# Kernel optimization log

Hardware: AMD Instinct MI355X
Metric: run time of the kernel (lower is better)

## Reference

```python
import jax, jax.numpy as jnp
import numpy as np

HID, NHEAD, NLAYERS = 128, 8, 6
BS, H, W = 1, 64, 128
HD = HID // NHEAD  # head dim = 16


def layer_norm(x, g, b, eps=1e-5):
    m = jnp.mean(x, -1, keepdims=True)
    v = jnp.mean((x - m) ** 2, -1, keepdims=True)
    return (x - m) * jax.lax.rsqrt(v + eps) * g + b


def mha_relative(query, kv, in_w, in_b, out_w, out_b, pos_enc, pos_idx, attn_mask, is_self):
    # query/kv: [W, N, C]; in_w: [3C, C]; pos_enc: [2W-1, C]; pos_idx: [W*W]
    w, n, c = query.shape
    if is_self:
        q, k, v = jnp.split(query @ in_w.T + in_b, 3, axis=-1)
    else:
        q = query @ in_w[:c].T + in_b[:c]
        k, v = jnp.split(kv @ in_w[c:].T + in_b[c:], 2, axis=-1)
    # relative positional bias: gather [2W-1,C] -> [W,W,C], project with q/k weights
    pos_sel = pos_enc[pos_idx].reshape(w, w, c)
    q_r, k_r = jnp.split(pos_sel @ in_w[:2 * c].T + in_b[:2 * c], 2, axis=-1)
    scale = HD ** -0.5
    q = (q * scale).reshape(w, n, NHEAD, HD)
    k = k.reshape(w, n, NHEAD, HD)
    v = v.reshape(w, n, NHEAD, HD)
    q_r = (q_r * scale).reshape(w, w, NHEAD, HD)
    k_r = k_r.reshape(w, w, NHEAD, HD)
    attn = (jnp.einsum('wnec,vnec->newv', q, k)
            + jnp.einsum('wnec,wvec->newv', q, k_r)
            + jnp.einsum('vnec,wvec->newv', k, q_r))  # [N,E,W,W]
    if attn_mask is not None:
        attn = attn + attn_mask[None, None]
    raw_attn = attn.sum(axis=1)  # [N,W,W] head-summed raw scores
    a = jax.nn.softmax(attn, axis=-1)
    v_o = jnp.einsum('newv,vnec->wnec', a, v).reshape(w, n, c)
    return v_o @ out_w.T + out_b, raw_attn


def setup_inputs() -> dict:
    key = jax.random.key(0)
    ks = jax.random.split(key, 8)
    f32 = jnp.float32
    s = 0.02
    d = {}
    d['feat_left'] = jax.random.normal(ks[0], (BS, HID, H, W), f32)
    d['feat_right'] = jax.random.normal(ks[1], (BS, HID, H, W), f32)
    d['pos_enc'] = jax.random.normal(ks[2], (2 * W - 1, HID), f32)
    d['self_ln_g'] = jnp.ones((NLAYERS, HID), f32)
    d['self_ln_b'] = jnp.zeros((NLAYERS, HID), f32)
    d['self_in_w'] = jax.random.normal(ks[3], (NLAYERS, 3 * HID, HID), f32) * s
    d['self_in_b'] = jnp.zeros((NLAYERS, 3 * HID), f32)
    d['self_out_w'] = jax.random.normal(ks[4], (NLAYERS, HID, HID), f32) * s
    d['self_out_b'] = jnp.zeros((NLAYERS, HID), f32)
    d['cross_ln1_g'] = jnp.ones((NLAYERS, HID), f32)
    d['cross_ln1_b'] = jnp.zeros((NLAYERS, HID), f32)
    d['cross_ln2_g'] = jnp.ones((NLAYERS, HID), f32)
    d['cross_ln2_b'] = jnp.zeros((NLAYERS, HID), f32)
    d['cross_in_w'] = jax.random.normal(ks[5], (NLAYERS, 3 * HID, HID), f32) * s
    d['cross_in_b'] = jnp.zeros((NLAYERS, 3 * HID), f32)
    d['cross_out_w'] = jax.random.normal(ks[6], (NLAYERS, HID, HID), f32) * s
    d['cross_out_b'] = jnp.zeros((NLAYERS, HID), f32)
    return d


def reference(feat_left, feat_right, pos_enc, self_ln_g, self_ln_b, self_in_w, self_in_b,
              self_out_w, self_out_b, cross_ln1_g, cross_ln1_b, cross_ln2_g, cross_ln2_b,
              cross_in_w, cross_in_b, cross_out_w, cross_out_b):
    bs, c, hn, w = feat_left.shape  # bs must be 1 (as in source)
    # [N,C,H,W] -> [W, H*N, C]
    fl = jnp.transpose(feat_left, (3, 2, 0, 1)).reshape(w, hn * bs, c)
    fr = jnp.transpose(feat_right, (3, 2, 0, 1)).reshape(w, hn * bs, c)
    HN = hn * bs
    # pos_indexes[i,j] = (w-1-i) + j, values in [0, 2w-2]
    pos_idx = ((w - 1 - jnp.arange(w))[:, None] + jnp.arange(w)[None, :]).reshape(-1)
    causal = jnp.triu(jnp.full((w, w), -jnp.inf, feat_left.dtype), k=1)
    feat = jnp.concatenate([fl, fr], axis=1)  # [W, 2HN, C]
    raw_attn = None
    for i in range(NLAYERS):
        # self attention over concatenated left+right rows
        f2 = layer_norm(feat, self_ln_g[i], self_ln_b[i])
        upd, _ = mha_relative(f2, f2, self_in_w[i], self_in_b[i], self_out_w[i],
                              self_out_b[i], pos_enc, pos_idx, None, True)
        feat = feat + upd
        left, right = feat[:, :HN], feat[:, HN:]
        # cross attention: left queries attend to norm2(right)
        # (source computes a right-update with norm1/flipped pos but discards it)
        l2 = layer_norm(left, cross_ln1_g[i], cross_ln1_b[i])
        r2 = layer_norm(right, cross_ln2_g[i], cross_ln2_b[i])
        mask = causal if i == NLAYERS - 1 else None
        upd, raw_attn = mha_relative(l2, r2, cross_in_w[i], cross_in_b[i], cross_out_w[i],
                                     cross_out_b[i], pos_enc, pos_idx, mask, False)
        left = left + upd
        feat = jnp.concatenate([left, right], axis=1)
    # [HN,W,W] -> [bs, hn, W, W]
    return jnp.transpose(raw_attn.reshape(hn, bs, w, w), (1, 0, 2, 3))
```

## Files before the change

### kernel.cpp

```cpp
#include <hip/hip_runtime.h>
#include <cmath>

#define CDIM 128

typedef __attribute__((ext_vector_type(8))) short bf16x8;
typedef __attribute__((ext_vector_type(4))) float f32x4;
typedef unsigned short u16;

__device__ inline unsigned pk2(float a, float b) {
    unsigned ua = __float_as_uint(a) + 0x8000u;
    unsigned ub = __float_as_uint(b) + 0x8000u;
    return (ua >> 16) | (ub & 0xffff0000u);
}
__device__ inline u16 pk1(float x) {
    return (u16)((__float_as_uint(x) + 0x8000u) >> 16);
}
__device__ inline float ubf(u16 u) { return __uint_as_float(((unsigned)u) << 16); }
__device__ inline float ulo(unsigned u) { return __uint_as_float(u << 16); }
__device__ inline float uhi(unsigned u) { return __uint_as_float(u & 0xffff0000u); }

__global__ __launch_bounds__(256) void setup1_kernel(const float* __restrict__ w0,
                                                     const float* __restrict__ w1,
                                                     const float* __restrict__ w2,
                                                     const float* __restrict__ w3,
                                                     const float* __restrict__ b0,
                                                     const float* __restrict__ b1,
                                                     u16* __restrict__ wout,
                                                     float* __restrict__ bout,
                                                     const float* __restrict__ FL,
                                                     const float* __restrict__ FR,
                                                     u16* __restrict__ feat) {
    __shared__ float t[32][33];
    int bb = blockIdx.x;
    if (bb < 786) {
        int idx = bb * 256 + threadIdx.x;
        if (idx < 196608) {
            const float* src; long off4; u16* dst;
            if (idx < 73728)       { src = w0; off4 = idx;           dst = wout; }
            else if (idx < 147456) { src = w1; off4 = idx - 73728;   dst = wout + 294912; }
            else if (idx < 172032) { src = w2; off4 = idx - 147456;  dst = wout + 589824; }
            else                   { src = w3; off4 = idx - 172032;  dst = wout + 688128; }
            float4 f = *(const float4*)(src + off4 * 4);
            *(uint2*)(dst + off4 * 4) = make_uint2(pk2(f.x, f.y), pk2(f.z, f.w));
        } else {
            int tt = idx - 196608;
            if (tt < 4608) bout[tt] = (tt < 2304) ? b0[tt] : b1[tt - 2304];
        }
        return;
    }
    int b = bb - 786;
    int cb = b & 3, wb = (b >> 2) & 3, n = b >> 4;
    const float* src = (n < 64) ? FL : FR;
    int nn = n & 63;
    int j = threadIdx.x & 31, i0 = threadIdx.x >> 5;
    #pragma unroll
    for (int p = 0; p < 4; p++) {
        int i = i0 + p * 8;
        t[i][j] = src[(cb * 32 + i) * 8192 + nn * 128 + wb * 32 + j];
    }
    __syncthreads();
    #pragma unroll
    for (int p = 0; p < 4; p++) {
        int i = i0 + p * 8;
        feat[((long)(wb * 32 + i) * 128 + n) * 128 + cb * 32 + j] = pk1(t[j][i]);
    }
}

__global__ __launch_bounds__(256, 4) void setup2_kernel(const u16* __restrict__ feat,
                                                        const float* __restrict__ g,
                                                        const float* __restrict__ b,
                                                        u16* __restrict__ lnB,
                                                        const float* __restrict__ Apos,
                                                        const u16* __restrict__ Wpp,
                                                        const float* __restrict__ biaspp,
                                                        u16* __restrict__ Cpp,
                                                        float scale) {
    __shared__ __align__(16) u16 sA[64 * 136];
    __shared__ __align__(16) u16 sW[64 * 136];
    int bb = blockIdx.x;
    int tid = threadIdx.x;
    if (bb < 1024) {
        int wv = tid >> 6, lane = tid & 63;
        float g0 = g[lane * 2], b0 = b[lane * 2];
        float g1 = g[lane * 2 + 1], b1 = b[lane * 2 + 1];
        #pragma unroll
        for (int rr = 0; rr < 4; rr++) {
            long m = (long)bb * 16 + wv * 4 + rr;
            unsigned u = *(const unsigned*)(feat + m * 128 + lane * 2);
            float x0 = ulo(u), x1 = uhi(u);
            float s = x0 + x1, q = x0 * x0 + x1 * x1;
            #pragma unroll
            for (int off = 1; off < 64; off <<= 1) {
                s += __shfl_xor(s, off);
                q += __shfl_xor(q, off);
            }
            float mean = s * (1.f / 128.f);
            float var = q * (1.f / 128.f) - mean * mean;
            float rs = rsqrtf(var + 1e-5f);
            float y0 = (x0 - mean) * rs * g0 + b0;
            float y1 = (x1 - mean) * rs * g1 + b1;
            *(unsigned*)(lnB + m * 128 + lane * 2) = pk2(y0, y1);
        }
        return;
    }
    int b2 = bb - 1024;
    int bx = b2 & 3, byy = (b2 >> 2) & 3, z = b2 >> 4;
    const int M = 255, N = 256;
    const u16* W = Wpp + (long)z * 49152;
    const float* bias = biaspp + z * 384;
    u16* C = Cpp + (long)z * 65280;
    int row0 = byy * 64, col0 = bx * 64;
    float4 zf4 = make_float4(0.f, 0.f, 0.f, 0.f);
    int kc = tid & 31;
    #pragma unroll
    for (int i = 0; i < 8; i++) {
        int r = (tid + i * 256) >> 5;
        int m = row0 + r;
        int jn = col0 + r;
        float4 fa = (m < M) ? *(const float4*)(Apos + (long)m * 128 + kc * 4) : zf4;
        uint2 uw = make_uint2(0u, 0u);
        if (jn < N) uw = *(const uint2*)(W + (long)jn * 128 + kc * 4);
        *(uint2*)&sA[r * 136 + kc * 4] = make_uint2(pk2(fa.x, fa.y), pk2(fa.z, fa.w));
        *(uint2*)&sW[r * 136 + kc * 4] = uw;
    }
    __syncthreads();

    int wv = tid >> 6, lane = tid & 63, quad = lane >> 4, col = lane & 15;
    f32x4 z4 = {0.f, 0.f, 0.f, 0.f};
    f32x4 acc0 = z4, acc1 = z4, acc2 = z4, acc3 = z4;
    #pragma unroll
    for (int kb = 0; kb < 4; kb++) {
        bf16x8 a = *(const bf16x8*)&sA[(wv * 16 + col) * 136 + kb * 32 + quad * 8];
        bf16x8 b0 = *(const bf16x8*)&sW[(0 * 16 + col) * 136 + kb * 32 + quad * 8];
        bf16x8 b1 = *(const bf16x8*)&sW[(1 * 16 + col) * 136 + kb * 32 + quad * 8];
        bf16x8 b2 = *(const bf16x8*)&sW[(2 * 16 + col) * 136 + kb * 32 + quad * 8];
        bf16x8 b3 = *(const bf16x8*)&sW[(3 * 16 + col) * 136 + kb * 32 + quad * 8];
        acc0 = __builtin_amdgcn_mfma_f32_16x16x32_bf16(a, b0, acc0, 0, 0, 0);
        acc1 = __builtin_amdgcn_mfma_f32_16x16x32_bf16(a, b1, acc1, 0, 0, 0);
        acc2 = __builtin_amdgcn_mfma_f32_16x16x32_bf16(a, b2, acc2, 0, 0, 0);
        acc3 = __builtin_amdgcn_mfma_f32_16x16x32_bf16(a, b3, acc3, 0, 0, 0);
    }
    int mrow = row0 + wv * 16 + quad * 4;
    #pragma unroll
    for (int tc = 0; tc < 4; tc++) {
        f32x4 acc = tc == 0 ? acc0 : tc == 1 ? acc1 : tc == 2 ? acc2 : acc3;
        int jn = col0 + tc * 16 + col;
        if (jn >= N) continue;
        float bs = bias[jn];
        float sc = (jn < 128) ? scale : 1.f;
        long db = ((long)(jn >> 4) * 255) * 16 + (jn & 15);
        #pragma unroll
        for (int reg = 0; reg < 4; reg++) {
            int m = mrow + reg;
            if (m >= M) continue;
            C[db + (long)m * 16] = pk1((acc[reg] + bs) * sc);
        }
    }
}

__global__ __launch_bounds__(256, 3) void gemm_qkv128_kernel(const u16* __restrict__ A,
                                                             const u16* __restrict__ W,
                                                             const float* __restrict__ bias,
                                                             u16* __restrict__ C,
                                                             float scale) {
    __shared__ __align__(16) u16 sA[128 * 136];
    __shared__ __align__(16) u16 sW[64 * 136];
    int tid = threadIdx.x;
    int row0 = blockIdx.y * 128, col0 = blockIdx.x * 64;
    int kc = tid & 31;
    #pragma unroll
    for (int i = 0; i < 16; i++) {
        int r = (tid + i * 256) >> 5;
        *(uint2*)&sA[r * 136 + kc * 4] =
            *(const uint2*)(A + (long)(row0 + r) * 128 + kc * 4);
    }
    #pragma unroll
    for (int i = 0; i < 8; i++) {
        int r = (tid + i * 256) >> 5;
        *(uint2*)&sW[r * 136 + kc * 4] =
            *(const uint2*)(W + (long)(col0 + r) * 128 + kc * 4);
    }
    __syncthreads();

    int wv = tid >> 6, lane = tid & 63, quad = lane >> 4, col = lane & 15;
    f32x4 z4 = {0.f, 0.f, 0.f, 0.f};
    f32x4 accA0 = z4, accA1 = z4, accA2 = z4, accA3 = z4;
    f32x4 accB0 = z4, accB1 = z4, accB2 = z4, accB3 = z4;
    #pragma unroll
    for (int kb = 0; kb < 4; kb++) {
        bf16x8 a0 = *(const bf16x8*)&sA[(wv * 32 + col) * 136 + kb * 32 + quad * 8];
        bf16x8 a1 = *(const bf16x8*)&sA[(wv * 32 + 16 + col) * 136 + kb * 32 + quad * 8];
        bf16x8 b0 = *(const bf16x8*)&sW[(0 * 16 + col) * 136 + kb * 32 + quad * 8];
        bf16x8 b1 = *(const bf16x8*)&sW[(1 * 16 + col) * 136 + kb * 32 + quad * 8];
        bf16x8 b2 = *(const bf16x8*)&sW[(2 * 16 + col) * 136 + kb * 32 + quad * 8];
        bf16x8 b3 = *(const bf16x8*)&sW[(3 * 16 + col) * 136 + kb * 32 + quad * 8];
        accA0 = __builtin_amdgcn_mfma_f32_16x16x32_bf16(a0, b0, accA0, 0, 0, 0);
        accA1 = __builtin_amdgcn_mfma_f32_16x16x32_bf16(a0, b1, accA1, 0, 0, 0);
        accA2 = __builtin_amdgcn_mfma_f32_16x16x32_bf16(a0, b2, accA2, 0, 0, 0);
        accA3 = __builtin_amdgcn_mfma_f32_16x16x32_bf16(a0, b3, accA3, 0, 0, 0);
        accB0 = __builtin_amdgcn_mfma_f32_16x16x32_bf16(a1, b0, accB0, 0, 0, 0);
        accB1 = __builtin_amdgcn_mfma_f32_16x16x32_bf16(a1, b1, accB1, 0, 0, 0);
        accB2 = __builtin_amdgcn_mfma_f32_16x16x32_bf16(a1, b2, accB2, 0, 0, 0);
        accB3 = __builtin_amdgcn_mfma_f32_16x16x32_bf16(a1, b3, accB3, 0, 0, 0);
    }
    long woff = (long)blockIdx.y * 16;
    #pragma unroll
    for (int st = 0; st < 2; st++) {
        int nrow = wv * 32 + st * 16 + quad * 4;
        #pragma unroll
        for (int tc = 0; tc < 4; tc++) {
            f32x4 acc;
            if (st == 0) acc = tc == 0 ? accA0 : tc == 1 ? accA1 : tc == 2 ? accA2 : accA3;
            else         acc = tc == 0 ? accB0 : tc == 1 ? accB1 : tc == 2 ? accB2 : accB3;
            int jn = col0 + tc * 16 + col;
            float bs = bias[jn];
            float sc = (jn < 128) ? scale : 1.f;
            long db = ((long)(jn >> 4) * 128) * 2048 + woff + (jn & 15);
            #pragma unroll
            for (int reg = 0; reg < 4; reg++)
                C[db + (long)(nrow + reg) * 2048] = pk1((acc[reg] + bs) * sc);
        }
    }
}

__global__ __launch_bounds__(256, 2) void f1_out_self_cqkv_kernel(
        const u16* __restrict__ A,
        const u16* __restrict__ W,
        const float* __restrict__ bias,
        u16* __restrict__ feat,
        const float* __restrict__ g1, const float* __restrict__ b1,
        const float* __restrict__ g2, const float* __restrict__ b2,
        const float* __restrict__ sng, const float* __restrict__ snb,
        u16* __restrict__ lnB,
        const u16* __restrict__ Wcr,
        const float* __restrict__ biac,
        u16* __restrict__ QKV,
        float scale) {
    __shared__ __align__(16) u16 sA[64 * 136];
    __shared__ __align__(16) u16 sW[128 * 136];
    int tid = threadIdx.x;
    int by = blockIdx.x;
    int row0 = by * 64;
    int right = by & 1;
    int w = by >> 1;
    int kc = tid & 31;
    #pragma unroll
    for (int i = 0; i < 8; i++) {
        int r = (tid + i * 256) >> 5;
        *(uint2*)&sA[r * 136 + kc * 4] = *(const uint2*)(A + (long)(row0 + r) * 128 + kc * 4);
    }
    #pragma unroll
    for (int i = 0; i < 16; i++) {
        int r = (tid + i * 256) >> 5;
        *(uint2*)&sW[r * 136 + kc * 4] = *(const uint2*)(W + (long)r * 128 + kc * 4);
    }
    __syncthreads();

    int wv = tid >> 6, lane = tid & 63, quad = lane >> 4, col = lane & 15;
    f32x4 acc[8] = {};
    #pragma unroll
    for (int kb = 0; kb < 4; kb++) {
        bf16x8 a = *(const bf16x8*)&sA[(wv * 16 + col) * 136 + kb * 32 + quad * 8];
        #pragma unroll
        for (int tc = 0; tc < 8; tc++) {
            bf16x8 b = *(const bf16x8*)&sW[(tc * 16 + col) * 136 + kb * 32 + quad * 8];
            acc[tc] = __builtin_amdgcn_mfma_f32_16x16x32_bf16(a, b, acc[tc], 0, 0, 0);
        }
    }
    __syncthreads();

    const float* gA = right ? g2 : g1;
    const float* bA = right ? b2 : b1;
    float gAv[8], bAv[8], gBv[8], bBv[8], bsv[8];
    bool doB = (sng != nullptr) && right;
    #pragma unroll
    for (int tc = 0; tc < 8; tc++) {
        int jn = tc * 16 + col;
        gAv[tc] = gA[jn]; bAv[tc] = bA[jn]; bsv[tc] = bias[jn];
        if (doB) { gBv[tc] = sng[jn]; bBv[tc] = snb[jn]; }
    }
    #pragma unroll
    for (int reg = 0; reg < 4; reg++) {
        int nloc = wv * 16 + quad * 4 + reg;
        long m = row0 + nloc;
        long rb = m * 128;
        float o[8];
        float s = 0.f, q = 0.f;
        #pragma unroll
        for (int tc = 0; tc < 8; tc++) {
            int jn = tc * 16 + col;
            float v = acc[tc][reg] + bsv[tc] + ubf(feat[rb + jn]);
            o[tc] = v; s += v; q += v * v;
        }
        #pragma unroll
        for (int off = 1; off < 16; off <<= 1) {
            s += __shfl_xor(s, off);
            q += __shfl_xor(q, off);
        }
        float mean = s * (1.f / 128.f);
        float var = q * (1.f / 128.f) - mean * mean;
        float rs = rsqrtf(var + 1e-5f);
        #pragma unroll
        for (int tc = 0; tc < 8; tc++) {
            int jn = tc * 16 + col;
            feat[rb + jn] = pk1(o[tc]);
            float ln = (o[tc] - mean) * rs;
            sA[nloc * 136 + jn] = pk1(ln * gAv[tc] + bAv[tc]);
            if (doB) lnB[rb + jn] = pk1(ln * gBv[tc] + bBv[tc]);
        }
    }
    __syncthreads();

    int passes = right ? 2 : 1;
    for (int p = 0; p < passes; p++) {
        if (p) __syncthreads();
        int wrow0 = right ? (128 + p * 128) : 0;
        #pragma unroll
        for (int i = 0; i < 16; i++) {
            int r = (tid + i * 256) >> 5;
            *(uint2*)&sW[r * 136 + kc * 4] =
                *(const uint2*)(Wcr + (long)(wrow0 + r) * 128 + kc * 4);
        }
        __syncthreads();
        f32x4 acb[8] = {};
        #pragma unroll
        for (int kb = 0; kb < 4; kb++) {
            bf16x8 a = *(const bf16x8*)&sA[(wv * 16 + col) * 136 + kb * 32 + quad * 8];
            #pragma unroll
            for (int tc = 0; tc < 8; tc++) {
                bf16x8 b = *(const bf16x8*)&sW[(tc * 16 + col) * 136 + kb * 32 + quad * 8];
                acb[tc] = __builtin_amdgcn_mfma_f32_16x16x32_bf16(a, b, acb[tc], 0, 0, 0);
            }
        }
        float sc = right ? 1.f : scale;
        int nrow = wv * 16 + quad * 4;
        #pragma unroll
        for (int tc = 0; tc < 8; tc++) {
            int jn = tc * 16 + col;
            float bs = biac[wrow0 + jn];
            int strip = right ? (8 + p * 8 + (jn >> 4)) : (jn >> 4);
            long db = (long)strip * 131072 + w * 16 + (jn & 15);
            #pragma unroll
            for (int reg = 0; reg < 4; reg++)
                QKV[db + (long)(nrow + reg) * 2048] = pk1((acb[tc][reg] + bs) * sc);
        }
    }
}

__global__ __launch_bounds__(256, 3) void gemm_out_cross_kernel(const u16* __restrict__ A,
                                                                const u16* __restrict__ W,
                                                                const float* __restrict__ bias,
                                                                u16* __restrict__ feat,
                                                                const float* __restrict__ sng,
                                                                const float* __restrict__ snb,
                                                                u16* __restrict__ lnB) {
    __shared__ __align__(16) u16 sA[64 * 136];
    __shared__ __align__(16) u16 sW[128 * 136];
    int tid = threadIdx.x;
    int row0 = blockIdx.x * 64;
    int kc = tid & 31;
    #pragma unroll
    for (int i = 0; i < 8; i++) {
        int r = (tid + i * 256) >> 5;
        *(uint2*)&sA[r * 136 + kc * 4] = *(const uint2*)(A + (long)(row0 + r) * 128 + kc * 4);
    }
    #pragma unroll
    for (int i = 0; i < 16; i++) {
        int r = (tid + i * 256) >> 5;
        *(uint2*)&sW[r * 136 + kc * 4] = *(const uint2*)(W + (long)r * 128 + kc * 4);
    }
    __syncthreads();

    int wv = tid >> 6, lane = tid & 63, quad = lane >> 4, col = lane & 15;
    f32x4 acc[8] = {};
    #pragma unroll
    for (int kb = 0; kb < 4; kb++) {
        bf16x8 a = *(const bf16x8*)&sA[(wv * 16 + col) * 136 + kb * 32 + quad * 8];
        #pragma unroll
        for (int tc = 0; tc < 8; tc++) {
            bf16x8 b = *(const bf16x8*)&sW[(tc * 16 + col) * 136 + kb * 32 + quad * 8];
            acc[tc] = __builtin_amdgcn_mfma_f32_16x16x32_bf16(a, b, acc[tc], 0, 0, 0);
        }
    }
    float gBv[8], bBv[8], bsv[8];
    #pragma unroll
    for (int tc = 0; tc < 8; tc++) {
        int jn = tc * 16 + col;
        gBv[tc] = sng[jn]; bBv[tc] = snb[jn]; bsv[tc] = bias[jn];
    }
    #pragma unroll
    for (int reg = 0; reg < 4; reg++) {
        long m = row0 + wv * 16 + quad * 4 + reg;
        long rb = ((m >> 6) * 128 + (m & 63)) * 128;
        float o[8];
        float s = 0.f, q = 0.f;
        #pragma unroll
        for (int tc = 0; tc < 8; tc++) {
            int jn = tc * 16 + col;
            float v = acc[tc][reg] + bsv[tc] + ubf(feat[rb + jn]);
            o[tc] = v; s += v; q += v * v;
        }
        #pragma unroll
        for (int off = 1; off < 16; off <<= 1) {
            s += __shfl_xor(s, off);
            q += __shfl_xor(q, off);
        }
        float mean = s * (1.f / 128.f);
        float var = q * (1.f / 128.f) - mean * mean;
        float rs = rsqrtf(var + 1e-5f);
        #pragma unroll
        for (int tc = 0; tc < 8; tc++) {
            int jn = tc * 16 + col;
            feat[rb + jn] = pk1(o[tc]);
            lnB[rb + jn] = pk1((o[tc] - mean) * rs * gBv[tc] + bBv[tc]);
        }
    }
}

__global__ __launch_bounds__(512, 8) void attn_kernel(const u16* __restrict__ QKV,
                                                      const u16* __restrict__ PPL,
                                                      u16* __restrict__ VO,
                                                      float* __restrict__ RAW,
                                                      int NN, int causal) {
    __shared__ __align__(16) u16 sm[19584];
    const int SKV = 0, SA = 2176;
    int e = blockIdx.x, n = blockIdx.y;
    int tid = threadIdx.x;
    int wv = tid >> 6, lane = tid & 63, quad = lane >> 4, col = lane & 15;

    const u16* qb = QKV + ((long)e * NN + n) * 2048;
    const u16* kb = QKV + ((long)(8 + e) * NN + n) * 2048;
    const u16* vb = QKV + ((long)(16 + e) * NN + n) * 2048;
    const u16* qr = PPL + (long)e * 4080;
    const u16* kr = PPL + (long)(8 + e) * 4080;

    bf16x8 zf = {0, 0, 0, 0, 0, 0, 0, 0};
    f32x4 z4 = {0.f, 0.f, 0.f, 0.f};
    bf16x8 aQ = zf, aK = zf;
    if (quad < 2) {
        aQ = *(const bf16x8*)(qb + (wv * 16 + col) * 16 + quad * 8);
        aK = *(const bf16x8*)(kb + (wv * 16 + col) * 16 + quad * 8);
    }
    {
        int row = tid >> 2, c = tid & 3;
        *(uint2*)&sm[SKV + row * 16 + c * 4] = *(const uint2*)(kb + row * 16 + c * 4);
    }
    __syncthreads();

    f32x4 s1[8];
    #pragma unroll
    for (int tv = 0; tv < 8; tv++) {
        bf16x8 b = zf;
        if (quad < 2) b = *(const bf16x8*)&sm[SKV + (tv * 16 + col) * 16 + quad * 8];
        s1[tv] = __builtin_amdgcn_mfma_f32_16x16x32_bf16(aQ, b, z4, 0, 0, 0);
    }
    int wbq = wv * 16 + quad * 4;
    int s2lo = 7 - wv;
    #pragma unroll 3
    for (int tt = 0; tt < 9; tt++) {
        int tr = s2lo + tt;
        bf16x8 b = zf;
        if (quad < 2) b = *(const bf16x8*)(kr + (tr * 16 + col) * 16 + quad * 8);
        f32x4 d = __builtin_amdgcn_mfma_f32_16x16x32_bf16(aQ, b, z4, 0, 0, 0);
        #pragma unroll
        for (int reg = 0; reg < 4; reg++) {
            int v = tr * 16 + col - 127 + wbq + reg;
            if (v >= 0 && v < 128) sm[SA + (wbq + reg) * 136 + v] = pk1(d[reg]);
        }
    }
    __syncthreads();
    {
        int row = tid >> 2, c = tid & 3;
        uint2 uv = *(const uint2*)(vb + row * 16 + c * 4);
        sm[SKV + (c * 4 + 0) * 136 + row] = (u16)(uv.x & 0xffffu);
        sm[SKV + (c * 4 + 1) * 136 + row] = (u16)(uv.x >> 16);
        sm[SKV + (c * 4 + 2) * 136 + row] = (u16)(uv.y & 0xffffu);
        sm[SKV + (c * 4 + 3) * 136 + row] = (u16)(uv.y >> 16);
    }
    #pragma unroll 3
    for (int tt = 0; tt < 9; tt++) {
        int tr = wv + tt;
        bf16x8 b = zf;
        if (quad < 2) b = *(const bf16x8*)(qr + (tr * 16 + col) * 16 + quad * 8);
        f32x4 d = __builtin_amdgcn_mfma_f32_16x16x32_bf16(aK, b, z4, 0, 0, 0);
        #pragma unroll
        for (int reg = 0; reg < 4; reg++) {
            int v = wbq + reg;
            int w = 127 + v - (tr * 16 + col);
            if (w >= 0 && w < 128) {
                int addr = SA + w * 136 + v;
                sm[addr] = pk1(ubf(sm[addr]) + d[reg]);
            }
        }
    }
    __syncthreads();

    float rs0 = 0.f, rs1 = 0.f, rs2 = 0.f, rs3 = 0.f;
    #pragma unroll
    for (int tv = 0; tv < 8; tv++) {
        f32x4 c = s1[tv];
        int v = tv * 16 + col;
        #pragma unroll
        for (int reg = 0; reg < 4; reg++) {
            int w = wbq + reg;
            int addr = SA + w * 136 + v;
            float a = c[reg] + ubf(sm[addr]);
            bool live = !(causal && v > w);
            float p = live ? __expf(a) : 0.f;
            if (RAW) RAW[(long)n * 16384 + w * 128 + v] = live ? a : 0.f;
            sm[addr] = pk1(p);
            if (reg == 0) rs0 += p; else if (reg == 1) rs1 += p;
            else if (reg == 2) rs2 += p; else rs3 += p;
        }
    }
    #pragma unroll
    for (int o = 1; o < 16; o <<= 1) {
        rs0 += __shfl_xor(rs0, o);
        rs1 += __shfl_xor(rs1, o);
        rs2 += __shfl_xor(rs2, o);
        rs3 += __shfl_xor(rs3, o);
    }
    __syncthreads();

    f32x4 o4 = z4;
    #pragma unroll
    for (int kb = 0; kb < 4; kb++) {
        bf16x8 a = *(const bf16x8*)&sm[SA + (wv * 16 + col) * 136 + kb * 32 + quad * 8];
        bf16x8 b = *(const bf16x8*)&sm[SKV + col * 136 + kb * 32 + quad * 8];
        o4 = __builtin_amdgcn_mfma_f32_16x16x32_bf16(a, b, o4, 0, 0, 0);
    }
    float iv0 = 1.f / rs0, iv1 = 1.f / rs1, iv2 = 1.f / rs2, iv3 = 1.f / rs3;
    VO[(long)((wbq + 0) * NN + n) * CDIM + e * 16 + col] = pk1(o4[0] * iv0);
    VO[(long)((wbq + 1) * NN + n) * CDIM + e * 16 + col] = pk1(o4[1] * iv1);
    VO[(long)((wbq + 2) * NN + n) * CDIM + e * 16 + col] = pk1(o4[2] * iv2);
    VO[(long)((wbq + 3) * NN + n) * CDIM + e * 16 + col] = pk1(o4[3] * iv3);
}

extern "C" void kernel_launch(void* const* d_in, const int* in_sizes, int n_in,
                              void* d_out, int out_size, void* d_ws, size_t ws_size,
                              hipStream_t stream) {
    const float* FL         = (const float*)d_in[0];
    const float* FR         = (const float*)d_in[1];
    const float* pos_enc    = (const float*)d_in[2];
    const float* self_ln_g  = (const float*)d_in[3];
    const float* self_ln_b  = (const float*)d_in[4];
    const float* self_in_w  = (const float*)d_in[5];
    const float* self_in_b  = (const float*)d_in[6];
    const float* self_out_w = (const float*)d_in[7];
    const float* self_out_b = (const float*)d_in[8];
    const float* cr_ln1_g   = (const float*)d_in[9];
    const float* cr_ln1_b   = (const float*)d_in[10];
    const float* cr_ln2_g   = (const float*)d_in[11];
    const float* cr_ln2_b   = (const float*)d_in[12];
    const float* cr_in_w    = (const float*)d_in[13];
    const float* cr_in_b    = (const float*)d_in[14];
    const float* cr_out_w   = (const float*)d_in[15];
    const float* cr_out_b   = (const float*)d_in[16];

    float* ws       = (float*)d_ws;
    u16*   feat     = (u16*)ws;
    u16*   vo       = (u16*)(ws + 1048576);
    u16*   qkvS     = (u16*)(ws + 2097152);
    u16*   pp_self  = (u16*)(ws + 5242880);
    u16*   pp_cross = pp_self + 391680;
    u16*   wbf      = (u16*)(ws + 5634560);
    u16*   wsel_in  = wbf;
    u16*   wcr_in   = wbf + 294912;
    u16*   wsel_out = wbf + 589824;
    u16*   wcr_out  = wbf + 688128;
    float* bin      = ws + 6027776;
    u16*   lnB      = (u16*)(ws + 7080960);
    float* out      = (float*)d_out;

    const float scale = 0.25f;

    setup1_kernel<<<2834, 256, 0, stream>>>(self_in_w, cr_in_w, self_out_w, cr_out_w,
                                            self_in_b, cr_in_b, wbf, bin,
                                            FL, FR, feat);
    setup2_kernel<<<1216, 256, 0, stream>>>(feat, self_ln_g, self_ln_b, lnB,
                                            pos_enc, wsel_in, bin, pp_self, scale);

    for (int i = 0; i < 6; i++) {
        int last = (i == 5);
        gemm_qkv128_kernel<<<dim3(6, 128), 256, 0, stream>>>(lnB, wsel_in + i * 49152,
                                                             self_in_b + i * 384, qkvS, scale);
        attn_kernel<<<dim3(8, 128), 512, 0, stream>>>(qkvS, pp_self + i * 65280,
                                                      vo, nullptr, 128, 0);
        f1_out_self_cqkv_kernel<<<256, 256, 0, stream>>>(vo, wsel_out + i * 16384,
                                                         self_out_b + i * 128, feat,
                                                         cr_ln1_g + i * 128, cr_ln1_b + i * 128,
                                                         cr_ln2_g + i * 128, cr_ln2_b + i * 128,
                                                         last ? nullptr : self_ln_g + (i + 1) * 128,
                                                         last ? nullptr : self_ln_b + (i + 1) * 128,
                                                         lnB,
                                                         wcr_in + i * 49152,
                                                         cr_in_b + i * 384,
                                                         qkvS, scale);

        attn_kernel<<<dim3(8, 64), 512, 0, stream>>>(qkvS, pp_cross + i * 65280,
                                                     vo, last ? out : nullptr,
                                                     64, last);
        if (!last) {
            gemm_out_cross_kernel<<<128, 256, 0, stream>>>(vo, wcr_out + i * 16384,
                                                           cr_out_b + i * 128, feat,
                                                           self_ln_g + (i + 1) * 128,
                                                           self_ln_b + (i + 1) * 128,
                                                           lnB);
        }
    }
}
```

Before: 484.0 us.

## Fuse cross out-proj with next layer's self QKV projection and prefetch weights

The cross-attention output projection plus LayerNorm is merged with the next layer's self-attention QKV GEMM into one kernel, so the separate per-layer gemm_qkv128 launch is removed after the first layer. Left-half blocks compute the output projection and LayerNorm into shared memory, and right-half blocks load the existing normalized rows, before both run the QKV projection. Weight tiles for upcoming GEMM passes are prefetched into registers while the current pass computes, in this kernel and in the f1 kernel. The aim is fewer launches and less global round-trip of the normalized activations, at the cost of higher register pressure (launch bounds reduced to 2 blocks) and of right-half blocks reading lnB values written by an earlier launch.

```diff
diff --git a/kernel.cpp b/kernel.cpp
--- a/kernel.cpp
+++ b/kernel.cpp
@@ -244,6 +244,7 @@
     int right = by & 1;
     int w = by >> 1;
     int kc = tid & 31;
+    uint2 pw[16];
     #pragma unroll
     for (int i = 0; i < 8; i++) {
         int r = (tid + i * 256) >> 5;
@@ -253,6 +254,14 @@
     for (int i = 0; i < 16; i++) {
         int r = (tid + i * 256) >> 5;
         *(uint2*)&sW[r * 136 + kc * 4] = *(const uint2*)(W + (long)r * 128 + kc * 4);
+    }
+    {
+        int w0 = right ? 128 : 0;
+        #pragma unroll
+        for (int i = 0; i < 16; i++) {
+            int r = (tid + i * 256) >> 5;
+            pw[i] = *(const uint2*)(Wcr + (long)(w0 + r) * 128 + kc * 4);
+        }
     }
     __syncthreads();
 
@@ -268,6 +277,19 @@
         }
     }
     __syncthreads();
+
+    #pragma unroll
+    for (int i = 0; i < 16; i++) {
+        int r = (tid + i * 256) >> 5;
+        *(uint2*)&sW[r * 136 + kc * 4] = pw[i];
+    }
+    if (right) {
+        #pragma unroll
+        for (int i = 0; i < 16; i++) {
+            int r = (tid + i * 256) >> 5;
+            pw[i] = *(const uint2*)(Wcr + (long)(256 + r) * 128 + kc * 4);
+        }
+    }
 
     const float* gA = right ? g2 : g1;
     const float* bA = right ? b2 : b1;
@@ -312,16 +334,19 @@
     __syncthreads();
 
     int passes = right ? 2 : 1;
-    for (int p = 0; p < passes; p++) {
-        if (p) __syncthreads();
+    #pragma unroll
+    for (int p = 0; p < 2; p++) {
+        if (p >= passes) break;
+        if (p) {
+            __syncthreads();
+            #pragma unroll
+            for (int i = 0; i < 16; i++) {
+                int r = (tid + i * 256) >> 5;
+                *(uint2*)&sW[r * 136 + kc * 4] = pw[i];
+            }
+            __syncthreads();
+        }
         int wrow0 = right ? (128 + p * 128) : 0;
-        #pragma unroll
-        for (int i = 0; i < 16; i++) {
-            int r = (tid + i * 256) >> 5;
-            *(uint2*)&sW[r * 136 + kc * 4] =
-                *(const uint2*)(Wcr + (long)(wrow0 + r) * 128 + kc * 4);
-        }
-        __syncthreads();
         f32x4 acb[8] = {};
         #pragma unroll
         for (int kb = 0; kb < 4; kb++) {
@@ -347,72 +372,150 @@
     }
 }
 
-__global__ __launch_bounds__(256, 3) void gemm_out_cross_kernel(const u16* __restrict__ A,
-                                                                const u16* __restrict__ W,
-                                                                const float* __restrict__ bias,
-                                                                u16* __restrict__ feat,
-                                                                const float* __restrict__ sng,
-                                                                const float* __restrict__ snb,
-                                                                u16* __restrict__ lnB) {
+__global__ __launch_bounds__(256, 2) void f2_out_cross_qkv_kernel(
+        const u16* __restrict__ A,
+        const u16* __restrict__ W,
+        const float* __restrict__ bias,
+        u16* __restrict__ feat,
+        const float* __restrict__ sng,
+        const float* __restrict__ snb,
+        const u16* __restrict__ lnBg,
+        const u16* __restrict__ Wsl,
+        const float* __restrict__ biasq,
+        u16* __restrict__ QKV,
+        float scale) {
     __shared__ __align__(16) u16 sA[64 * 136];
     __shared__ __align__(16) u16 sW[128 * 136];
     int tid = threadIdx.x;
-    int row0 = blockIdx.x * 64;
+    int t = blockIdx.x;
+    int right = t & 1, w = t >> 1;
     int kc = tid & 31;
-    #pragma unroll
-    for (int i = 0; i < 8; i++) {
-        int r = (tid + i * 256) >> 5;
-        *(uint2*)&sA[r * 136 + kc * 4] = *(const uint2*)(A + (long)(row0 + r) * 128 + kc * 4);
+    uint2 pw[16];
+    if (!right) {
+        #pragma unroll
+        for (int i = 0; i < 8; i++) {
+            int r = (tid + i * 256) >> 5;
+            *(uint2*)&sA[r * 136 + kc * 4] =
+                *(const uint2*)(A + (long)(w * 64 + r) * 128 + kc * 4);
+        }
+        #pragma unroll
+        for (int i = 0; i < 16; i++) {
+            int r = (tid + i * 256) >> 5;
+            *(uint2*)&sW[r * 136 + kc * 4] = *(const uint2*)(W + (long)r * 128 + kc * 4);
+        }
+    } else {
+        #pragma unroll
+        for (int i = 0; i < 8; i++) {
+            int r = (tid + i * 256) >> 5;
+            *(uint2*)&sA[r * 136 + kc * 4] =
+                *(const uint2*)(lnBg + (long)(w * 128 + 64 + r) * 128 + kc * 4);
+        }
     }
     #pragma unroll
     for (int i = 0; i < 16; i++) {
         int r = (tid + i * 256) >> 5;
-        *(uint2*)&sW[r * 136 + kc * 4] = *(const uint2*)(W + (long)r * 128 + kc * 4);
+        pw[i] = *(const uint2*)(Wsl + (long)r * 128 + kc * 4);
     }
     __syncthreads();
 
     int wv = tid >> 6, lane = tid & 63, quad = lane >> 4, col = lane & 15;
-    f32x4 acc[8] = {};
-    #pragma unroll
-    for (int kb = 0; kb < 4; kb++) {
-        bf16x8 a = *(const bf16x8*)&sA[(wv * 16 + col) * 136 + kb * 32 + quad * 8];
-        #pragma unroll
-        for (int tc = 0; tc < 8; tc++) {
-            bf16x8 b = *(const bf16x8*)&sW[(tc * 16 + col) * 136 + kb * 32 + quad * 8];
-            acc[tc] = __builtin_amdgcn_mfma_f32_16x16x32_bf16(a, b, acc[tc], 0, 0, 0);
-        }
-    }
-    float gBv[8], bBv[8], bsv[8];
-    #pragma unroll
-    for (int tc = 0; tc < 8; tc++) {
-        int jn = tc * 16 + col;
-        gBv[tc] = sng[jn]; bBv[tc] = snb[jn]; bsv[tc] = bias[jn];
-    }
-    #pragma unroll
-    for (int reg = 0; reg < 4; reg++) {
-        long m = row0 + wv * 16 + quad * 4 + reg;
-        long rb = ((m >> 6) * 128 + (m & 63)) * 128;
-        float o[8];
-        float s = 0.f, q = 0.f;
+    if (!right) {
+        f32x4 acc[8] = {};
+        #pragma unroll
+        for (int kb = 0; kb < 4; kb++) {
+            bf16x8 a = *(const bf16x8*)&sA[(wv * 16 + col) * 136 + kb * 32 + quad * 8];
+            #pragma unroll
+            for (int tc = 0; tc < 8; tc++) {
+                bf16x8 b = *(const bf16x8*)&sW[(tc * 16 + col) * 136 + kb * 32 + quad * 8];
+                acc[tc] = __builtin_amdgcn_mfma_f32_16x16x32_bf16(a, b, acc[tc], 0, 0, 0);
+            }
+        }
+        __syncthreads();
+        float gBv[8], bBv[8], bsv[8];
         #pragma unroll
         for (int tc = 0; tc < 8; tc++) {
             int jn = tc * 16 + col;
-            float v = acc[tc][reg] + bsv[tc] + ubf(feat[rb + jn]);
-            o[tc] = v; s += v; q += v * v;
-        }
-        #pragma unroll
-        for (int off = 1; off < 16; off <<= 1) {
-            s += __shfl_xor(s, off);
-            q += __shfl_xor(q, off);
-        }
-        float mean = s * (1.f / 128.f);
-        float var = q * (1.f / 128.f) - mean * mean;
-        float rs = rsqrtf(var + 1e-5f);
+            gBv[tc] = sng[jn]; bBv[tc] = snb[jn]; bsv[tc] = bias[jn];
+        }
+        #pragma unroll
+        for (int reg = 0; reg < 4; reg++) {
+            int nloc = wv * 16 + quad * 4 + reg;
+            long rb = ((long)w * 128 + nloc) * 128;
+            float o[8];
+            float s = 0.f, q = 0.f;
+            #pragma unroll
+            for (int tc = 0; tc < 8; tc++) {
+                int jn = tc * 16 + col;
+                float v = acc[tc][reg] + bsv[tc] + ubf(feat[rb + jn]);
+                o[tc] = v; s += v; q += v * v;
+            }
+            #pragma unroll
+            for (int off = 1; off < 16; off <<= 1) {
+                s += __shfl_xor(s, off);
+                q += __shfl_xor(q, off);
+            }
+            float mean = s * (1.f / 128.f);
+            float var = q * (1.f / 128.f) - mean * mean;
+            float rs = rsqrtf(var + 1e-5f);
+            #pragma unroll
+            for (int tc = 0; tc < 8; tc++) {
+                int jn = tc * 16 + col;
+                feat[rb + jn] = pk1(o[tc]);
+                sA[nloc * 136 + jn] = pk1((o[tc] - mean) * rs * gBv[tc] + bBv[tc]);
+            }
+        }
+    }
+    #pragma unroll
+    for (int i = 0; i < 16; i++) {
+        int r = (tid + i * 256) >> 5;
+        *(uint2*)&sW[r * 136 + kc * 4] = pw[i];
+    }
+    #pragma unroll
+    for (int i = 0; i < 16; i++) {
+        int r = (tid + i * 256) >> 5;
+        pw[i] = *(const uint2*)(Wsl + (long)(128 + r) * 128 + kc * 4);
+    }
+    __syncthreads();
+
+    int n0 = right ? 64 : 0;
+    #pragma unroll
+    for (int p = 0; p < 3; p++) {
+        if (p) {
+            __syncthreads();
+            #pragma unroll
+            for (int i = 0; i < 16; i++) {
+                int r = (tid + i * 256) >> 5;
+                *(uint2*)&sW[r * 136 + kc * 4] = pw[i];
+            }
+            if (p < 2) {
+                #pragma unroll
+                for (int i = 0; i < 16; i++) {
+                    int r = (tid + i * 256) >> 5;
+                    pw[i] = *(const uint2*)(Wsl + (long)(256 + r) * 128 + kc * 4);
+                }
+            }
+            __syncthreads();
+        }
+        f32x4 ac[8] = {};
+        #pragma unroll
+        for (int kb = 0; kb < 4; kb++) {
+            bf16x8 a = *(const bf16x8*)&sA[(wv * 16 + col) * 136 + kb * 32 + quad * 8];
+            #pragma unroll
+            for (int tc = 0; tc < 8; tc++) {
+                bf16x8 b = *(const bf16x8*)&sW[(tc * 16 + col) * 136 + kb * 32 + quad * 8];
+                ac[tc] = __builtin_amdgcn_mfma_f32_16x16x32_bf16(a, b, ac[tc], 0, 0, 0);
+            }
+        }
+        int nrow = n0 + wv * 16 + quad * 4;
         #pragma unroll
         for (int tc = 0; tc < 8; tc++) {
-            int jn = tc * 16 + col;
-            feat[rb + jn] = pk1(o[tc]);
-            lnB[rb + jn] = pk1((o[tc] - mean) * rs * gBv[tc] + bBv[tc]);
+            int jn = p * 128 + tc * 16 + col;
+            float bs = biasq[jn];
+            float sc = (jn < 128) ? scale : 1.f;
+            long db = (long)(jn >> 4) * 262144 + w * 16 + (jn & 15);
+            #pragma unroll
+            for (int reg = 0; reg < 4; reg++)
+                QKV[db + (long)(nrow + reg) * 2048] = pk1((ac[tc][reg] + bs) * sc);
         }
     }
 }
@@ -579,11 +682,11 @@
                                             FL, FR, feat);
     setup2_kernel<<<1216, 256, 0, stream>>>(feat, self_ln_g, self_ln_b, lnB,
                                             pos_enc, wsel_in, bin, pp_self, scale);
+    gemm_qkv128_kernel<<<dim3(6, 128), 256, 0, stream>>>(lnB, wsel_in,
+                                                         self_in_b, qkvS, scale);
 
     for (int i = 0; i < 6; i++) {
         int last = (i == 5);
-        gemm_qkv128_kernel<<<dim3(6, 128), 256, 0, stream>>>(lnB, wsel_in + i * 49152,
-                                                             self_in_b + i * 384, qkvS, scale);
         attn_kernel<<<dim3(8, 128), 512, 0, stream>>>(qkvS, pp_self + i * 65280,
                                                       vo, nullptr, 128, 0);
         f1_out_self_cqkv_kernel<<<256, 256, 0, stream>>>(vo, wsel_out + i * 16384,
@@ -601,11 +704,14 @@
                                                      vo, last ? out : nullptr,
                                                      64, last);
         if (!last) {
-            gemm_out_cross_kernel<<<128, 256, 0, stream>>>(vo, wcr_out + i * 16384,
-                                                           cr_out_b + i * 128, feat,
-                                                           self_ln_g + (i + 1) * 128,
-                                                           self_ln_b + (i + 1) * 128,
-                                                           lnB);
-        }
-    }
-}
+            f2_out_cross_qkv_kernel<<<256, 256, 0, stream>>>(vo, wcr_out + i * 16384,
+                                                             cr_out_b + i * 128, feat,
+                                                             self_ln_g + (i + 1) * 128,
+                                                             self_ln_b + (i + 1) * 128,
+                                                             lnB,
+                                                             wsel_in + (i + 1) * 49152,
+                                                             self_in_b + (i + 1) * 384,
+                                                             qkvS, scale);
+        }
+    }
+}
```

New measurement: 480.9 us. No clear change (-0.6%).

## Fuse cross out-projection with next layer's self QKV GEMM; drop LDS weight staging

Applied to the files above, without the earlier changes.

Merges the cross-attention output projection, residual and next-layer LayerNorm with the following self-attention QKV projection into one kernel. This removes the separate QKV GEMM launch per layer, except for the first, which is hoisted before the loop. Both fused GEMM kernels now read A and W operands straight from global memory into MFMA registers instead of staging them in shared memory. That cuts LDS use and barriers but depends on cache hits for the repeated weight reads. The right-half blocks read the already-normalized rows from the lnB buffer, while the left-half blocks recompute them.

```diff
diff --git a/kernel.cpp b/kernel.cpp
--- a/kernel.cpp
+++ b/kernel.cpp
@@ -237,37 +237,24 @@
         u16* __restrict__ QKV,
         float scale) {
     __shared__ __align__(16) u16 sA[64 * 136];
-    __shared__ __align__(16) u16 sW[128 * 136];
     int tid = threadIdx.x;
     int by = blockIdx.x;
     int row0 = by * 64;
     int right = by & 1;
     int w = by >> 1;
-    int kc = tid & 31;
-    #pragma unroll
-    for (int i = 0; i < 8; i++) {
-        int r = (tid + i * 256) >> 5;
-        *(uint2*)&sA[r * 136 + kc * 4] = *(const uint2*)(A + (long)(row0 + r) * 128 + kc * 4);
-    }
-    #pragma unroll
-    for (int i = 0; i < 16; i++) {
-        int r = (tid + i * 256) >> 5;
-        *(uint2*)&sW[r * 136 + kc * 4] = *(const uint2*)(W + (long)r * 128 + kc * 4);
-    }
-    __syncthreads();
-
     int wv = tid >> 6, lane = tid & 63, quad = lane >> 4, col = lane & 15;
+    int koff = quad * 8;
+
     f32x4 acc[8] = {};
     #pragma unroll
     for (int kb = 0; kb < 4; kb++) {
-        bf16x8 a = *(const bf16x8*)&sA[(wv * 16 + col) * 136 + kb * 32 + quad * 8];
+        bf16x8 a = *(const bf16x8*)(A + (long)(row0 + wv * 16 + col) * 128 + kb * 32 + koff);
         #pragma unroll
         for (int tc = 0; tc < 8; tc++) {
-            bf16x8 b = *(const bf16x8*)&sW[(tc * 16 + col) * 136 + kb * 32 + quad * 8];
+            bf16x8 b = *(const bf16x8*)(W + (long)(tc * 16 + col) * 128 + kb * 32 + koff);
             acc[tc] = __builtin_amdgcn_mfma_f32_16x16x32_bf16(a, b, acc[tc], 0, 0, 0);
         }
     }
-    __syncthreads();
 
     const float* gA = right ? g2 : g1;
     const float* bA = right ? b2 : b1;
@@ -311,29 +298,25 @@
     }
     __syncthreads();
 
+    bf16x8 pa[4];
+    #pragma unroll
+    for (int kb = 0; kb < 4; kb++)
+        pa[kb] = *(const bf16x8*)&sA[(wv * 16 + col) * 136 + kb * 32 + koff];
+
     int passes = right ? 2 : 1;
+    float sc = right ? 1.f : scale;
+    int nrow = wv * 16 + quad * 4;
     for (int p = 0; p < passes; p++) {
-        if (p) __syncthreads();
         int wrow0 = right ? (128 + p * 128) : 0;
-        #pragma unroll
-        for (int i = 0; i < 16; i++) {
-            int r = (tid + i * 256) >> 5;
-            *(uint2*)&sW[r * 136 + kc * 4] =
-                *(const uint2*)(Wcr + (long)(wrow0 + r) * 128 + kc * 4);
-        }
-        __syncthreads();
         f32x4 acb[8] = {};
         #pragma unroll
         for (int kb = 0; kb < 4; kb++) {
-            bf16x8 a = *(const bf16x8*)&sA[(wv * 16 + col) * 136 + kb * 32 + quad * 8];
             #pragma unroll
             for (int tc = 0; tc < 8; tc++) {
-                bf16x8 b = *(const bf16x8*)&sW[(tc * 16 + col) * 136 + kb * 32 + quad * 8];
-                acb[tc] = __builtin_amdgcn_mfma_f32_16x16x32_bf16(a, b, acb[tc], 0, 0, 0);
-            }
-        }
-        float sc = right ? 1.f : scale;
-        int nrow = wv * 16 + quad * 4;
+                bf16x8 b = *(const bf16x8*)(Wcr + (long)(wrow0 + tc * 16 + col) * 128 + kb * 32 + koff);
+                acb[tc] = __builtin_amdgcn_mfma_f32_16x16x32_bf16(pa[kb], b, acb[tc], 0, 0, 0);
+            }
+        }
         #pragma unroll
         for (int tc = 0; tc < 8; tc++) {
             int jn = tc * 16 + col;
@@ -347,72 +330,102 @@
     }
 }
 
-__global__ __launch_bounds__(256, 3) void gemm_out_cross_kernel(const u16* __restrict__ A,
-                                                                const u16* __restrict__ W,
-                                                                const float* __restrict__ bias,
-                                                                u16* __restrict__ feat,
-                                                                const float* __restrict__ sng,
-                                                                const float* __restrict__ snb,
-                                                                u16* __restrict__ lnB) {
+__global__ __launch_bounds__(256, 2) void f2_out_cross_qkv_kernel(
+        const u16* __restrict__ A,
+        const u16* __restrict__ W,
+        const float* __restrict__ bias,
+        u16* __restrict__ feat,
+        const float* __restrict__ sng,
+        const float* __restrict__ snb,
+        const u16* __restrict__ lnBg,
+        const u16* __restrict__ Wsl,
+        const float* __restrict__ biasq,
+        u16* __restrict__ QKV,
+        float scale) {
     __shared__ __align__(16) u16 sA[64 * 136];
-    __shared__ __align__(16) u16 sW[128 * 136];
     int tid = threadIdx.x;
-    int row0 = blockIdx.x * 64;
-    int kc = tid & 31;
-    #pragma unroll
-    for (int i = 0; i < 8; i++) {
-        int r = (tid + i * 256) >> 5;
-        *(uint2*)&sA[r * 136 + kc * 4] = *(const uint2*)(A + (long)(row0 + r) * 128 + kc * 4);
-    }
-    #pragma unroll
-    for (int i = 0; i < 16; i++) {
-        int r = (tid + i * 256) >> 5;
-        *(uint2*)&sW[r * 136 + kc * 4] = *(const uint2*)(W + (long)r * 128 + kc * 4);
-    }
-    __syncthreads();
-
+    int t = blockIdx.x;
+    int right = t & 1, w = t >> 1;
     int wv = tid >> 6, lane = tid & 63, quad = lane >> 4, col = lane & 15;
-    f32x4 acc[8] = {};
-    #pragma unroll
-    for (int kb = 0; kb < 4; kb++) {
-        bf16x8 a = *(const bf16x8*)&sA[(wv * 16 + col) * 136 + kb * 32 + quad * 8];
-        #pragma unroll
-        for (int tc = 0; tc < 8; tc++) {
-            bf16x8 b = *(const bf16x8*)&sW[(tc * 16 + col) * 136 + kb * 32 + quad * 8];
-            acc[tc] = __builtin_amdgcn_mfma_f32_16x16x32_bf16(a, b, acc[tc], 0, 0, 0);
-        }
-    }
-    float gBv[8], bBv[8], bsv[8];
-    #pragma unroll
-    for (int tc = 0; tc < 8; tc++) {
-        int jn = tc * 16 + col;
-        gBv[tc] = sng[jn]; bBv[tc] = snb[jn]; bsv[tc] = bias[jn];
-    }
-    #pragma unroll
-    for (int reg = 0; reg < 4; reg++) {
-        long m = row0 + wv * 16 + quad * 4 + reg;
-        long rb = ((m >> 6) * 128 + (m & 63)) * 128;
-        float o[8];
-        float s = 0.f, q = 0.f;
+    int koff = quad * 8;
+
+    bf16x8 pa[4];
+    if (!right) {
+        f32x4 acc[8] = {};
+        #pragma unroll
+        for (int kb = 0; kb < 4; kb++) {
+            bf16x8 a = *(const bf16x8*)(A + (long)(w * 64 + wv * 16 + col) * 128 + kb * 32 + koff);
+            #pragma unroll
+            for (int tc = 0; tc < 8; tc++) {
+                bf16x8 b = *(const bf16x8*)(W + (long)(tc * 16 + col) * 128 + kb * 32 + koff);
+                acc[tc] = __builtin_amdgcn_mfma_f32_16x16x32_bf16(a, b, acc[tc], 0, 0, 0);
+            }
+        }
+        float gBv[8], bBv[8], bsv[8];
         #pragma unroll
         for (int tc = 0; tc < 8; tc++) {
             int jn = tc * 16 + col;
-            float v = acc[tc][reg] + bsv[tc] + ubf(feat[rb + jn]);
-            o[tc] = v; s += v; q += v * v;
-        }
-        #pragma unroll
-        for (int off = 1; off < 16; off <<= 1) {
-            s += __shfl_xor(s, off);
-            q += __shfl_xor(q, off);
-        }
-        float mean = s * (1.f / 128.f);
-        float var = q * (1.f / 128.f) - mean * mean;
-        float rs = rsqrtf(var + 1e-5f);
+            gBv[tc] = sng[jn]; bBv[tc] = snb[jn]; bsv[tc] = bias[jn];
+        }
+        #pragma unroll
+        for (int reg = 0; reg < 4; reg++) {
+            int nloc = wv * 16 + quad * 4 + reg;
+            long rb = ((long)w * 128 + nloc) * 128;
+            float o[8];
+            float s = 0.f, q = 0.f;
+            #pragma unroll
+            for (int tc = 0; tc < 8; tc++) {
+                int jn = tc * 16 + col;
+                float v = acc[tc][reg] + bsv[tc] + ubf(feat[rb + jn]);
+                o[tc] = v; s += v; q += v * v;
+            }
+            #pragma unroll
+            for (int off = 1; off < 16; off <<= 1) {
+                s += __shfl_xor(s, off);
+                q += __shfl_xor(q, off);
+            }
+            float mean = s * (1.f / 128.f);
+            float var = q * (1.f / 128.f) - mean * mean;
+            float rs = rsqrtf(var + 1e-5f);
+            #pragma unroll
+            for (int tc = 0; tc < 8; tc++) {
+                int jn = tc * 16 + col;
+                feat[rb + jn] = pk1(o[tc]);
+                sA[nloc * 136 + jn] = pk1((o[tc] - mean) * rs * gBv[tc] + bBv[tc]);
+            }
+        }
+        __syncthreads();
+        #pragma unroll
+        for (int kb = 0; kb < 4; kb++)
+            pa[kb] = *(const bf16x8*)&sA[(wv * 16 + col) * 136 + kb * 32 + koff];
+    } else {
+        #pragma unroll
+        for (int kb = 0; kb < 4; kb++)
+            pa[kb] = *(const bf16x8*)(lnBg + (long)(w * 128 + 64 + wv * 16 + col) * 128 + kb * 32 + koff);
+    }
+
+    int n0 = right ? 64 : 0;
+    int nrow0 = n0 + wv * 16 + quad * 4;
+    #pragma unroll
+    for (int p = 0; p < 3; p++) {
+        f32x4 ac[8] = {};
+        #pragma unroll
+        for (int kb = 0; kb < 4; kb++) {
+            #pragma unroll
+            for (int tc = 0; tc < 8; tc++) {
+                bf16x8 b = *(const bf16x8*)(Wsl + (long)(p * 128 + tc * 16 + col) * 128 + kb * 32 + koff);
+                ac[tc] = __builtin_amdgcn_mfma_f32_16x16x32_bf16(pa[kb], b, ac[tc], 0, 0, 0);
+            }
+        }
         #pragma unroll
         for (int tc = 0; tc < 8; tc++) {
-            int jn = tc * 16 + col;
-            feat[rb + jn] = pk1(o[tc]);
-            lnB[rb + jn] = pk1((o[tc] - mean) * rs * gBv[tc] + bBv[tc]);
+            int jn = p * 128 + tc * 16 + col;
+            float bs = biasq[jn];
+            float sc = (jn < 128) ? scale : 1.f;
+            long db = (long)(jn >> 4) * 262144 + w * 16 + (jn & 15);
+            #pragma unroll
+            for (int reg = 0; reg < 4; reg++)
+                QKV[db + (long)(nrow0 + reg) * 2048] = pk1((ac[tc][reg] + bs) * sc);
         }
     }
 }
@@ -579,11 +592,11 @@
                                             FL, FR, feat);
     setup2_kernel<<<1216, 256, 0, stream>>>(feat, self_ln_g, self_ln_b, lnB,
                                             pos_enc, wsel_in, bin, pp_self, scale);
+    gemm_qkv128_kernel<<<dim3(6, 128), 256, 0, stream>>>(lnB, wsel_in,
+                                                         self_in_b, qkvS, scale);
 
     for (int i = 0; i < 6; i++) {
         int last = (i == 5);
-        gemm_qkv128_kernel<<<dim3(6, 128), 256, 0, stream>>>(lnB, wsel_in + i * 49152,
-                                                             self_in_b + i * 384, qkvS, scale);
         attn_kernel<<<dim3(8, 128), 512, 0, stream>>>(qkvS, pp_self + i * 65280,
                                                       vo, nullptr, 128, 0);
         f1_out_self_cqkv_kernel<<<256, 256, 0, stream>>>(vo, wsel_out + i * 16384,
@@ -601,11 +614,14 @@
                                                      vo, last ? out : nullptr,
                                                      64, last);
         if (!last) {
-            gemm_out_cross_kernel<<<128, 256, 0, stream>>>(vo, wcr_out + i * 16384,
-                                                           cr_out_b + i * 128, feat,
-                                                           self_ln_g + (i + 1) * 128,
-                                                           self_ln_b + (i + 1) * 128,
-                                                           lnB);
-        }
-    }
-}
+            f2_out_cross_qkv_kernel<<<256, 256, 0, stream>>>(vo, wcr_out + i * 16384,
+                                                             cr_out_b + i * 128, feat,
+                                                             self_ln_g + (i + 1) * 128,
+                                                             self_ln_b + (i + 1) * 128,
+                                                             lnB,
+                                                             wsel_in + (i + 1) * 49152,
+                                                             self_in_b + (i + 1) * 384,
+                                                             qkvS, scale);
+        }
+    }
+}
```

Result: slower. 544.9 us (+12.6%).
